# Optimization experiments

Hardware: AMD Instinct MI355X
Metric: run time of the kernel (lower is better)

The kernel has to match this reference:

```python
import jax, jax.numpy as jnp
import numpy as np
from jax import lax

D_MODEL, D_INNER, D_CONV, D_STATE, DT_RANK = 1024, 2048, 4, 16, 64
B, L = 2, 1024


def setup_inputs() -> dict:
    key = jax.random.key(0)
    ks = jax.random.split(key, 10)
    s = 0.02
    return {
        "x": jax.random.normal(ks[0], (B, L, D_MODEL), jnp.float32),
        "in_proj_w": jax.random.normal(ks[1], (2 * D_INNER, D_MODEL), jnp.float32) * s,
        "conv_w": jax.random.normal(ks[2], (D_INNER, 1, D_CONV), jnp.float32) * 0.1,
        "conv_b": jax.random.normal(ks[3], (D_INNER,), jnp.float32) * s,
        "x_proj_w": jax.random.normal(ks[4], (DT_RANK + 2 * D_STATE, D_INNER), jnp.float32) * s,
        "dt_proj_w": jax.random.normal(ks[5], (D_INNER, DT_RANK), jnp.float32) * s,
        "dt_proj_b": jax.random.normal(ks[6], (D_INNER,), jnp.float32) * s,
        "A_log": jnp.log(jnp.broadcast_to(jnp.arange(1, D_STATE + 1, dtype=jnp.float32), (D_INNER, D_STATE))),
        "D": jax.random.normal(ks[7], (D_INNER,), jnp.float32),
        "out_proj_w": jax.random.normal(ks[8], (D_MODEL, D_INNER), jnp.float32) * s,
    }


def _silu(v):
    return v * jax.nn.sigmoid(v)


def reference(x, in_proj_w, conv_w, conv_b, x_proj_w, dt_proj_w, dt_proj_b, A_log, D, out_proj_w):
    # in_proj: [B,L,d_model] -> [B,L,2*d_inner], split into x and gate z
    xz = jnp.einsum("bld,ed->ble", x, in_proj_w)
    xi, z = jnp.split(xz, 2, axis=-1)  # each [B,L,d_inner]

    # depthwise causal conv1d (padding = d_conv-1 on the left, output length L)
    xc = jnp.transpose(xi, (0, 2, 1))  # [B, d_inner, L]
    xc = lax.conv_general_dilated(
        xc, conv_w, window_strides=(1,), padding=[(D_CONV - 1, 0)],
        feature_group_count=D_INNER, dimension_numbers=("NCH", "OIH", "NCH"))
    xc = xc + conv_b[None, :, None]
    xc = _silu(jnp.transpose(xc, (0, 2, 1)))  # [B,L,d_inner]

    # selective scan parameters
    x_dbl = jnp.einsum("bld,ed->ble", xc, x_proj_w)  # [B,L,dt_rank+2*d_state]
    dt, Bm, Cm = jnp.split(x_dbl, [DT_RANK, DT_RANK + D_STATE], axis=-1)
    delta = jax.nn.softplus(jnp.einsum("blr,dr->bld", dt, dt_proj_w) + dt_proj_b)  # [B,L,d_inner]
    A = -jnp.exp(A_log)  # [d_inner, d_state]

    deltaA = jnp.exp(delta[..., None] * A)                       # [B,L,d_inner,N]
    deltaBu = delta[..., None] * Bm[:, :, None, :] * xc[..., None]  # [B,L,d_inner,N]

    def step(h, inp):
        a, bu, c = inp
        h = a * h + bu                         # [B,d_inner,N]
        y = jnp.einsum("bdn,bn->bd", h, c)     # [B,d_inner]
        return h, y

    h0 = jnp.zeros((x.shape[0], D_INNER, D_STATE), xc.dtype)
    _, ys = lax.scan(step, h0, (jnp.moveaxis(deltaA, 1, 0),
                                jnp.moveaxis(deltaBu, 1, 0),
                                jnp.moveaxis(Cm, 1, 0)))
    y = jnp.moveaxis(ys, 0, 1)  # [B,L,d_inner]

    y = y + xc * D
    y = y * _silu(z)
    return jnp.einsum("bld,ed->ble", y, out_proj_w)  # [B,L,d_model]
```

## Files before the change

kernel.cpp:

```cpp
#include <hip/hip_runtime.h>
#include <math.h>
#include <stdint.h>

#define DMODEL 1024
#define DINNER 2048
#define DCONV  4
#define DSTATE 16
#define DTRANK 64
#define BB 2
#define LL 1024
#define MM (BB * LL)

#define CL  64
#define NCH (LL / CL)

#define AS1(p) ((__attribute__((address_space(1))) void*)(void*)(p))
#define AS3(p) ((__attribute__((address_space(3))) void*)(void*)(p))

typedef __attribute__((ext_vector_type(8))) short bf16x8;
typedef __attribute__((ext_vector_type(4))) float f32x4;

__device__ __forceinline__ ushort bf16_rne(float f) {
  uint32_t u = __float_as_uint(f);
  uint32_t r = (u + 0x7fffu + ((u >> 16) & 1u)) >> 16;
  return (ushort)r;
}

__device__ __forceinline__ void split4(const float* __restrict__ in,
                                       ushort* __restrict__ hi,
                                       ushort* __restrict__ lo, int i4) {
  const float4 v = *reinterpret_cast<const float4*>(in + (size_t)i4 * 4);
  ushort4 h;
  h.x = bf16_rne(v.x); h.y = bf16_rne(v.y);
  h.z = bf16_rne(v.z); h.w = bf16_rne(v.w);
  *reinterpret_cast<ushort4*>(hi + (size_t)i4 * 4) = h;
  if (lo) {
    ushort4 l;
    l.x = bf16_rne(v.x - __uint_as_float((uint)h.x << 16));
    l.y = bf16_rne(v.y - __uint_as_float((uint)h.y << 16));
    l.z = bf16_rne(v.z - __uint_as_float((uint)h.z << 16));
    l.w = bf16_rne(v.w - __uint_as_float((uint)h.w << 16));
    *reinterpret_cast<ushort4*>(lo + (size_t)i4 * 4) = l;
  }
}

__global__ __launch_bounds__(256)
void split3(const float* s0, ushort* h0, ushort* l0, int n0,
            const float* s1, ushort* h1, ushort* l1, int n1,
            const float* s2, ushort* h2, ushort* l2, int n2,
            const float* s3, ushort* h3, ushort* l3, int n3) {
  int i = blockIdx.x * 256 + threadIdx.x;
  if (i < n0) { split4(s0, h0, l0, i); return; }
  i -= n0;
  if (i < n1) { split4(s1, h1, l1, i); return; }
  i -= n1;
  if (i < n2) { split4(s2, h2, l2, i); return; }
  i -= n2;
  if (i < n3) { split4(s3, h3, l3, i); return; }
}

__device__ __forceinline__ int swz4(int r) { return (r & 3) ^ ((r >> 2) & 3); }

template<int EPI, int SPLITK>
__global__ __launch_bounds__(256)
void gemm_hl_mfma(const ushort* __restrict__ Ahg, const ushort* __restrict__ Alg,
                  const ushort* __restrict__ Bhg, const ushort* __restrict__ Blg,
                  float* __restrict__ C, const float* __restrict__ bias,
                  int M, int N, int K) {
  __shared__ ushort Ah[2][128][32];
  __shared__ ushort Al[2][128][32];
  __shared__ ushort Bh[2][128][32];
  __shared__ ushort Bl[2][128][32];

  const int tid  = threadIdx.x;
  const int wave = tid >> 6;
  const int lane = tid & 63;
  const int m0 = blockIdx.y * 128;
  const int n0 = blockIdx.x * 128;
  const int wm = (wave >> 1) * 64;
  const int wn = (wave & 1) * 64;

  const int ksl = K / SPLITK;
  const int kb  = blockIdx.z * ksl;
  float* Cout   = C + (size_t)blockIdx.z * M * N;

  f32x4 acc[4][4];
  #pragma unroll
  for (int i = 0; i < 4; ++i)
    #pragma unroll
    for (int j = 0; j < 4; ++j)
      acc[i][j] = (f32x4){0.f, 0.f, 0.f, 0.f};

  const ushort* gsrc; ushort* dst; int row0;
  if      (wave == 0) { gsrc = Ahg; dst = &Ah[0][0][0]; row0 = m0; }
  else if (wave == 1) { gsrc = Alg; dst = &Al[0][0][0]; row0 = m0; }
  else if (wave == 2) { gsrc = Bhg; dst = &Bh[0][0][0]; row0 = n0; }
  else                { gsrc = Blg; dst = &Bl[0][0][0]; row0 = n0; }

  const int lr = lane >> 2;
  const int ls = lane & 3;
  const int fr = lane & 15;
  const int q  = lane >> 4;

  auto STAGE = [&](int bi, int k0) {
    ushort* d = dst + bi * 4096;
    #pragma unroll
    for (int seg = 0; seg < 8; ++seg) {
      const int rho = seg * 16 + lr;
      const int ks  = (ls ^ swz4(rho)) * 8;
      __builtin_amdgcn_global_load_lds(
          AS1(gsrc + (size_t)(row0 + rho) * K + k0 + ks),
          AS3(d + seg * 512), 16, 0, 0);
    }
  };

  const int NT = ksl / 32;
  STAGE(0, kb);
  __syncthreads();

  int cur = 0;
  for (int kt = 0; kt < NT; ++kt) {
    if (kt + 1 < NT) STAGE(cur ^ 1, kb + (kt + 1) * 32);

    bf16x8 ah[4], al[4], bh[4], bl[4];
    #pragma unroll
    for (int f = 0; f < 4; ++f) {
      { const int r = wm + f * 16 + fr; const int s = 8 * (q ^ swz4(r));
        ah[f] = *reinterpret_cast<const bf16x8*>(&Ah[cur][r][s]);
        al[f] = *reinterpret_cast<const bf16x8*>(&Al[cur][r][s]); }
      { const int r = wn + f * 16 + fr; const int s = 8 * (q ^ swz4(r));
        bh[f] = *reinterpret_cast<const bf16x8*>(&Bh[cur][r][s]);
        bl[f] = *reinterpret_cast<const bf16x8*>(&Bl[cur][r][s]); }
    }
    #pragma unroll
    for (int i = 0; i < 4; ++i)
      #pragma unroll
      for (int j = 0; j < 4; ++j) {
        acc[i][j] = __builtin_amdgcn_mfma_f32_16x16x32_bf16(ah[i], bh[j], acc[i][j], 0, 0, 0);
        acc[i][j] = __builtin_amdgcn_mfma_f32_16x16x32_bf16(al[i], bh[j], acc[i][j], 0, 0, 0);
        acc[i][j] = __builtin_amdgcn_mfma_f32_16x16x32_bf16(ah[i], bl[j], acc[i][j], 0, 0, 0);
      }

    __syncthreads();
    cur ^= 1;
  }

  const int cr = (lane >> 4) * 4;
  const int cc = lane & 15;
  #pragma unroll
  for (int i = 0; i < 4; ++i)
    #pragma unroll
    for (int j = 0; j < 4; ++j) {
      const int cn = n0 + wn + j * 16 + cc;
      const float bj = (EPI == 1) ? bias[cn] : 0.f;
      const size_t base = (size_t)(m0 + wm + i * 16 + cr) * N + cn;
      #pragma unroll
      for (int r = 0; r < 4; ++r) {
        float v = acc[i][j][r];
        if (EPI == 1) {
          v += bj;
          v = fmaxf(v, 0.f) + __logf(1.f + __expf(-fabsf(v)));
        }
        Cout[base + (size_t)r * N] = v;
      }
    }
}

template<int EPI, int SPLITK>
__global__ __launch_bounds__(256)
void gemm_p1_mfma(const ushort* __restrict__ Ahg, const ushort* __restrict__ Bhg,
                  float* __restrict__ P, int M, int N, int K) {
  __shared__ ushort Ah[2][128][32];
  __shared__ ushort Bh[2][128][32];

  const int tid  = threadIdx.x;
  const int wave = tid >> 6;
  const int lane = tid & 63;
  const int m0 = blockIdx.y * 128;
  const int n0 = blockIdx.x * 128;
  const int wm = (wave >> 1) * 64;
  const int wn = (wave & 1) * 64;

  const int ksl = K / SPLITK;
  const int kb  = blockIdx.z * ksl;
  float* Cout   = P + (size_t)blockIdx.z * M * N;

  f32x4 acc[4][4];
  #pragma unroll
  for (int i = 0; i < 4; ++i)
    #pragma unroll
    for (int j = 0; j < 4; ++j)
      acc[i][j] = (f32x4){0.f, 0.f, 0.f, 0.f};

  const ushort* gsrc = nullptr; ushort* dst = nullptr; int row0 = 0;
  if      (wave == 0) { gsrc = Ahg; dst = &Ah[0][0][0]; row0 = m0; }
  else if (wave == 1) { gsrc = Bhg; dst = &Bh[0][0][0]; row0 = n0; }

  const int lr = lane >> 2;
  const int ls = lane & 3;
  const int fr = lane & 15;
  const int q  = lane >> 4;

  auto STAGE = [&](int bi, int k0) {
    if (wave >= 2) return;
    ushort* d = dst + bi * 4096;
    #pragma unroll
    for (int seg = 0; seg < 8; ++seg) {
      const int rho = seg * 16 + lr;
      const int ks  = (ls ^ swz4(rho)) * 8;
      __builtin_amdgcn_global_load_lds(
          AS1(gsrc + (size_t)(row0 + rho) * K + k0 + ks),
          AS3(d + seg * 512), 16, 0, 0);
    }
  };

  const int NT = ksl / 32;
  STAGE(0, kb);
  __syncthreads();

  int cur = 0;
  for (int kt = 0; kt < NT; ++kt) {
    if (kt + 1 < NT) STAGE(cur ^ 1, kb + (kt + 1) * 32);

    bf16x8 ah[4], bh[4];
    #pragma unroll
    for (int f = 0; f < 4; ++f) {
      { const int r = wm + f * 16 + fr; const int s = 8 * (q ^ swz4(r));
        ah[f] = *reinterpret_cast<const bf16x8*>(&Ah[cur][r][s]); }
      { const int r = wn + f * 16 + fr; const int s = 8 * (q ^ swz4(r));
        bh[f] = *reinterpret_cast<const bf16x8*>(&Bh[cur][r][s]); }
    }
    #pragma unroll
    for (int i = 0; i < 4; ++i)
      #pragma unroll
      for (int j = 0; j < 4; ++j)
        acc[i][j] = __builtin_amdgcn_mfma_f32_16x16x32_bf16(ah[i], bh[j], acc[i][j], 0, 0, 0);

    __syncthreads();
    cur ^= 1;
  }

  const int cr = (lane >> 4) * 4;
  const int cc = lane & 15;
  #pragma unroll
  for (int i = 0; i < 4; ++i)
    #pragma unroll
    for (int j = 0; j < 4; ++j) {
      const int cn = n0 + wn + j * 16 + cc;
      const size_t base = (size_t)(m0 + wm + i * 16 + cr) * N + cn;
      #pragma unroll
      for (int r = 0; r < 4; ++r) {
        float v = acc[i][j][r];
        if (EPI == 2 && cn >= DINNER)
          v = v / (1.f + __expf(-v));
        Cout[base + (size_t)r * N] = v;
      }
    }
}

__global__ __launch_bounds__(256)
void splitk_reduce4(const float* __restrict__ P, float* __restrict__ out, int n) {
  const int i = (blockIdx.x * 256 + threadIdx.x) * 4;
  if (i >= n) return;
  float4 s = *reinterpret_cast<const float4*>(P + i);
  #pragma unroll
  for (int z = 1; z < 4; ++z) {
    const float4 v = *reinterpret_cast<const float4*>(P + (size_t)z * n + i);
    s.x += v.x; s.y += v.y; s.z += v.z; s.w += v.w;
  }
  *reinterpret_cast<float4*>(out + i) = s;
}

template<int BM, int BN, int TM, int TN, int KSLICE>
__global__ __launch_bounds__(256)
void gemm_nt_part(const float* __restrict__ A, const float* __restrict__ Bw,
                  float* __restrict__ P, int M, int N, int lda, int ldb) {
  constexpr int BK  = 16;
  constexpr int NTX = BN / TN;
  constexpr int NTY = BM / TM;
  static_assert(NTX * NTY == 256, "thread tile mismatch");
  __shared__ float As[BK][BM + 4];
  __shared__ float Bs[BK][BN + 4];

  const int tid = threadIdx.x;
  const int m0  = blockIdx.y * BM;
  const int n0  = blockIdx.x * BN;
  const int kb  = blockIdx.z * KSLICE;
  const int tx  = tid % NTX;
  const int ty  = tid / NTX;

  float acc[TM][TN] = {};

  for (int k0 = kb; k0 < kb + KSLICE; k0 += BK) {
    __syncthreads();
    for (int t = tid; t < BM * 4; t += 256) {
      const int row = t >> 2, kq = t & 3;
      const float4 v = *reinterpret_cast<const float4*>(
          A + (size_t)(m0 + row) * lda + k0 + kq * 4);
      As[kq * 4 + 0][row] = v.x;
      As[kq * 4 + 1][row] = v.y;
      As[kq * 4 + 2][row] = v.z;
      As[kq * 4 + 3][row] = v.w;
    }
    for (int t = tid; t < BN * 4; t += 256) {
      const int row = t >> 2, kq = t & 3;
      const float4 v = *reinterpret_cast<const float4*>(
          Bw + (size_t)(n0 + row) * ldb + k0 + kq * 4);
      Bs[kq * 4 + 0][row] = v.x;
      Bs[kq * 4 + 1][row] = v.y;
      Bs[kq * 4 + 2][row] = v.z;
      Bs[kq * 4 + 3][row] = v.w;
    }
    __syncthreads();
    #pragma unroll
    for (int k = 0; k < BK; ++k) {
      float a[TM], b[TN];
      #pragma unroll
      for (int i = 0; i < TM; ++i) a[i] = As[k][ty * TM + i];
      #pragma unroll
      for (int j = 0; j < TN; ++j) b[j] = Bs[k][tx * TN + j];
      #pragma unroll
      for (int i = 0; i < TM; ++i)
        #pragma unroll
        for (int j = 0; j < TN; ++j)
          acc[i][j] = fmaf(a[i], b[j], acc[i][j]);
    }
  }

  float* out = P + (size_t)blockIdx.z * M * N;
  #pragma unroll
  for (int i = 0; i < TM; ++i)
    #pragma unroll
    for (int j = 0; j < TN; ++j)
      out[(size_t)(m0 + ty * TM + i) * N + n0 + tx * TN + j] = acc[i][j];
}

__global__ __launch_bounds__(256)
void xpr_fused(const float* __restrict__ part, float* __restrict__ xdbl,
               ushort* __restrict__ dth, ushort* __restrict__ dtl) {
  const int i = blockIdx.x * 256 + threadIdx.x;
  if (i >= MM * 24) return;
  const int m  = i / 24;
  const int c4 = (i % 24) * 4;
  const size_t off = (size_t)m * 96 + c4;
  float4 s = *reinterpret_cast<const float4*>(part + off);
  #pragma unroll
  for (int z = 1; z < 8; ++z) {
    const float4 v = *reinterpret_cast<const float4*>(part + (size_t)z * MM * 96 + off);
    s.x += v.x; s.y += v.y; s.z += v.z; s.w += v.w;
  }
  if (c4 < 64) {
    ushort4 h, l;
    h.x = bf16_rne(s.x); l.x = bf16_rne(s.x - __uint_as_float((uint)h.x << 16));
    h.y = bf16_rne(s.y); l.y = bf16_rne(s.y - __uint_as_float((uint)h.y << 16));
    h.z = bf16_rne(s.z); l.z = bf16_rne(s.z - __uint_as_float((uint)h.z << 16));
    h.w = bf16_rne(s.w); l.w = bf16_rne(s.w - __uint_as_float((uint)h.w << 16));
    *reinterpret_cast<ushort4*>(dth + (size_t)m * 64 + c4) = h;
    *reinterpret_cast<ushort4*>(dtl + (size_t)m * 64 + c4) = l;
  } else {
    *reinterpret_cast<float4*>(xdbl + off) = s;
  }
}

__global__ __launch_bounds__(256)
void conv_silu(const float* __restrict__ xz, const float* __restrict__ cw,
               const float* __restrict__ cb, float* __restrict__ xc) {
  const int idx = blockIdx.x * 256 + threadIdx.x;
  if (idx >= MM * DINNER / 4) return;
  const int d4 = (idx & 511) * 4;
  const int m  = idx >> 9;
  const int l  = m & (LL - 1);
  const int b  = m >> 10;

  float4 w0 = *reinterpret_cast<const float4*>(cw + (size_t)(d4 + 0) * 4);
  float4 w1 = *reinterpret_cast<const float4*>(cw + (size_t)(d4 + 1) * 4);
  float4 w2 = *reinterpret_cast<const float4*>(cw + (size_t)(d4 + 2) * 4);
  float4 w3 = *reinterpret_cast<const float4*>(cw + (size_t)(d4 + 3) * 4);
  float4 acc = *reinterpret_cast<const float4*>(cb + d4);

  #pragma unroll
  for (int j = 0; j < DCONV; ++j) {
    const int ll = l - (DCONV - 1) + j;
    if (ll >= 0) {
      const float4 xv = *reinterpret_cast<const float4*>(
          xz + ((size_t)(b * LL + ll) << 12) + d4);
      acc.x = fmaf(xv.x, (&w0.x)[j], acc.x);
      acc.y = fmaf(xv.y, (&w1.x)[j], acc.y);
      acc.z = fmaf(xv.z, (&w2.x)[j], acc.z);
      acc.w = fmaf(xv.w, (&w3.x)[j], acc.w);
    }
  }
  float4 o;
  o.x = acc.x / (1.f + __expf(-acc.x));
  o.y = acc.y / (1.f + __expf(-acc.y));
  o.z = acc.z / (1.f + __expf(-acc.z));
  o.w = acc.w / (1.f + __expf(-acc.w));
  *reinterpret_cast<float4*>(xc + (size_t)m * DINNER + d4) = o;
}

__device__ __forceinline__ void stage_tile(const float* g, int stride,
                                           float* ldst, int lane) {
  const int r  = lane >> 2;
  const int q4 = (lane & 3) * 4;
  #pragma unroll
  for (int i = 0; i < 4; ++i) {
    __builtin_amdgcn_global_load_lds(
        AS1(g + (size_t)(i * 16 + r) * stride + q4),
        AS3(ldst + i * 256), 16, 0, 0);
  }
}

__device__ __forceinline__ float quad_sum(float v) {
  int i = __float_as_int(v);
  v += __int_as_float(__builtin_amdgcn_update_dpp(0, i, 0xB1, 0xf, 0xf, true));
  i = __float_as_int(v);
  v += __int_as_float(__builtin_amdgcn_update_dpp(0, i, 0x4E, 0xf, 0xf, true));
  return v;
}

__global__ __launch_bounds__(64)
void scan_chunk_state(const float* __restrict__ delta, const float* __restrict__ xc,
                      const float* __restrict__ xdbl, const float* __restrict__ A_log,
                      float* __restrict__ hend, float* __restrict__ aprod) {
  __shared__ float dT[CL][16];
  __shared__ float xT[CL][16];
  __shared__ float bT[CL][16];

  const int idx = blockIdx.x;
  const int c  = idx & 15;
  const int dg = (idx >> 4) & 127;
  const int b  = idx >> 11;
  const int t  = threadIdx.x;
  const int ch = t >> 2;
  const int q  = t & 3;
  const int d  = dg * 16 + ch;

  const size_t r0 = (size_t)b * LL + (size_t)c * CL;
  stage_tile(delta + r0 * DINNER + dg * 16, DINNER, &dT[0][0], t);
  stage_tile(xc    + r0 * DINNER + dg * 16, DINNER, &xT[0][0], t);
  stage_tile(xdbl  + r0 * 96 + DTRANK,          96, &bT[0][0], t);

  float Adn[4];
  #pragma unroll
  for (int j = 0; j < 4; ++j)
    Adn[j] = -__expf(A_log[d * DSTATE + 4 * q + j]);
  float h0 = 0.f, h1 = 0.f, h2 = 0.f, h3 = 0.f;
  float p0 = 1.f, p1 = 1.f, p2 = 1.f, p3 = 1.f;

  __syncthreads();

  #pragma unroll 8
  for (int l = 0; l < CL; ++l) {
    const float dv = dT[l][ch];
    const float xv = xT[l][ch];
    const float4 B4 = *reinterpret_cast<const float4*>(&bT[l][4 * q]);
    const float dvx = dv * xv;
    const float a0 = __expf(dv * Adn[0]);
    const float a1 = __expf(dv * Adn[1]);
    const float a2 = __expf(dv * Adn[2]);
    const float a3 = __expf(dv * Adn[3]);
    h0 = fmaf(a0, h0, dvx * B4.x);  p0 *= a0;
    h1 = fmaf(a1, h1, dvx * B4.y);  p1 *= a1;
    h2 = fmaf(a2, h2, dvx * B4.z);  p2 *= a2;
    h3 = fmaf(a3, h3, dvx * B4.w);  p3 *= a3;
  }

  const size_t base = (((size_t)(b * NCH + c) * DINNER) + d) * DSTATE + 4 * q;
  *reinterpret_cast<float4*>(hend  + base) = (float4){h0, h1, h2, h3};
  *reinterpret_cast<float4*>(aprod + base) = (float4){p0, p1, p2, p3};
}

__global__ __launch_bounds__(256)
void scan_combine(const float* __restrict__ hend, const float* __restrict__ aprod,
                  float* __restrict__ hin) {
  const int tid = blockIdx.x * 256 + threadIdx.x;
  const size_t cstride = (size_t)DINNER * DSTATE;
  const size_t base = (size_t)(tid >> 15) * NCH * cstride + (tid & 32767);
  float h = 0.f;
  hin[base] = 0.f;
  #pragma unroll
  for (int c = 0; c < NCH - 1; ++c) {
    h = fmaf(aprod[base + (size_t)c * cstride], h, hend[base + (size_t)c * cstride]);
    hin[base + (size_t)(c + 1) * cstride] = h;
  }
}

__global__ __launch_bounds__(64)
void scan_apply(const float* __restrict__ delta, const float* __restrict__ xc,
                const float* __restrict__ xdbl, const float* __restrict__ xz,
                const float* __restrict__ A_log, const float* __restrict__ Dp,
                const float* __restrict__ hin, ushort* __restrict__ yh) {
  __shared__ float dT[CL][16];
  __shared__ float xT[CL][16];
  __shared__ float bT[CL][16];
  __shared__ float cT[CL][16];
  __shared__ float zT[CL][16];

  const int idx = blockIdx.x;
  const int c  = idx & 15;
  const int dg = (idx >> 4) & 127;
  const int b  = idx >> 11;
  const int t  = threadIdx.x;
  const int ch = t >> 2;
  const int q  = t & 3;
  const int d  = dg * 16 + ch;

  const size_t r0 = (size_t)b * LL + (size_t)c * CL;
  stage_tile(delta + r0 * DINNER + dg * 16, DINNER, &dT[0][0], t);
  stage_tile(xc    + r0 * DINNER + dg * 16, DINNER, &xT[0][0], t);
  stage_tile(xdbl  + r0 * 96 + DTRANK,          96, &bT[0][0], t);
  stage_tile(xdbl  + r0 * 96 + DTRANK + DSTATE, 96, &cT[0][0], t);
  stage_tile(xz    + (r0 << 12) + DINNER + dg * 16, 4096, &zT[0][0], t);

  float Adn[4];
  #pragma unroll
  for (int j = 0; j < 4; ++j)
    Adn[j] = -__expf(A_log[d * DSTATE + 4 * q + j]);
  const float Dd = Dp[d];

  const size_t base = (((size_t)(b * NCH + c) * DINNER) + d) * DSTATE + 4 * q;
  const float4 h4 = *reinterpret_cast<const float4*>(hin + base);
  float h0 = h4.x, h1 = h4.y, h2 = h4.z, h3 = h4.w;

  __syncthreads();

  #pragma unroll 8
  for (int l = 0; l < CL; ++l) {
    const float dv = dT[l][ch];
    const float xv = xT[l][ch];
    const float4 B4 = *reinterpret_cast<const float4*>(&bT[l][4 * q]);
    const float4 C4 = *reinterpret_cast<const float4*>(&cT[l][4 * q]);
    const float dvx = dv * xv;
    const float a0 = __expf(dv * Adn[0]);
    const float a1 = __expf(dv * Adn[1]);
    const float a2 = __expf(dv * Adn[2]);
    const float a3 = __expf(dv * Adn[3]);
    h0 = fmaf(a0, h0, dvx * B4.x);
    h1 = fmaf(a1, h1, dvx * B4.y);
    h2 = fmaf(a2, h2, dvx * B4.z);
    h3 = fmaf(a3, h3, dvx * B4.w);
    float ys = fmaf(h0, C4.x, fmaf(h1, C4.y, fmaf(h2, C4.z, h3 * C4.w)));
    ys = quad_sum(ys);
    if (q == 0) {
      const float g = zT[l][ch];
      const float tv = (ys + xv * Dd) * g;
      yh[(r0 + l) * (size_t)DINNER + d] = bf16_rne(tv);
    }
  }
}

extern "C" void kernel_launch(void* const* d_in, const int* in_sizes, int n_in,
                              void* d_out, int out_size, void* d_ws, size_t ws_size,
                              hipStream_t stream) {
  const float* x         = (const float*)d_in[0];
  const float* in_proj_w = (const float*)d_in[1];
  const float* conv_w    = (const float*)d_in[2];
  const float* conv_b    = (const float*)d_in[3];
  const float* x_proj_w  = (const float*)d_in[4];
  const float* dt_proj_w = (const float*)d_in[5];
  const float* dt_proj_b = (const float*)d_in[6];
  const float* A_log     = (const float*)d_in[7];
  const float* Dv        = (const float*)d_in[8];
  const float* out_proj_w= (const float*)d_in[9];
  float* out = (float*)d_out;

  float* ws    = (float*)d_ws;
  float* xz    = ws;
  float* xc    = xz    + (size_t)MM * 4096;
  float* xdbl  = xc    + (size_t)MM * DINNER;
  float* delta = xdbl  + (size_t)MM * 96;
  ushort* us   = (ushort*)(delta + (size_t)MM * DINNER);
  ushort* yhp  = us;
  ushort* ylp  = yhp + (size_t)MM * DINNER;
  ushort* xh   = ylp + (size_t)MM * DINNER;
  ushort* xl   = xh  + (size_t)MM * DMODEL;
  ushort* wih  = xl  + (size_t)MM * DMODEL;
  ushort* wil  = wih + (size_t)4096 * DMODEL;
  ushort* woh  = wil + (size_t)4096 * DMODEL;

  ushort* dth = ylp;
  ushort* dtl = ylp + 131072;
  ushort* wdh = ylp + 262144;
  ushort* wdl = ylp + 393216;

  float* hend  = (float*)wih;
  float* aprod = hend  + (size_t)BB * NCH * DINNER * DSTATE;
  float* hin   = aprod + (size_t)BB * NCH * DINNER * DSTATE;
  float* part  = hend;
  float* opart = xz;

  const dim3 blk(256);

  {
    const int n0 = (MM * DMODEL) / 4, n1 = (4096 * DMODEL) / 4,
              n2 = (DMODEL * DINNER) / 4, n3 = (DINNER * DTRANK) / 4;
    split3<<<dim3((n0 + n1 + n2 + n3) / 256), blk, 0, stream>>>(
        x, xh, nullptr, n0, in_proj_w, wih, nullptr, n1,
        out_proj_w, woh, nullptr, n2, dt_proj_w, wdh, wdl, n3);
  }

  gemm_p1_mfma<2,1><<<dim3(4096 / 128, MM / 128), blk, 0, stream>>>(
      xh, wih, xz, MM, 4096, DMODEL);

  conv_silu<<<dim3((MM * DINNER / 4) / 256), blk, 0, stream>>>(xz, conv_w, conv_b, xc);

  gemm_nt_part<64,32,4,2,256><<<dim3(96/32, MM/64, 8), blk, 0, stream>>>(
      xc, x_proj_w, part, MM, 96, DINNER, DINNER);
  xpr_fused<<<dim3((MM * 24 + 255) / 256), blk, 0, stream>>>(part, xdbl, dth, dtl);

  gemm_hl_mfma<1,1><<<dim3(DINNER / 128, MM / 128), blk, 0, stream>>>(
      dth, dtl, wdh, wdl, delta, dt_proj_b, MM, DINNER, DTRANK);

  scan_chunk_state<<<dim3(BB * 128 * NCH), dim3(64), 0, stream>>>(
      delta, xc, xdbl, A_log, hend, aprod);
  scan_combine<<<dim3(BB * DINNER * DSTATE / 256), blk, 0, stream>>>(
      hend, aprod, hin);
  scan_apply<<<dim3(BB * 128 * NCH), dim3(64), 0, stream>>>(
      delta, xc, xdbl, xz, A_log, Dv, hin, yhp);

  gemm_p1_mfma<0,4><<<dim3(DMODEL / 128, MM / 128, 4), blk, 0, stream>>>(
      yhp, woh, opart, MM, DMODEL, DINNER);
  splitk_reduce4<<<dim3((MM * DMODEL) / 1024), blk, 0, stream>>>(
      opart, out, MM * DMODEL);
}
```

Measured before the change: 167.5 us.

## Store in_proj output as bf16 and coalesce GEMM epilogue via LDS transpose

The in_proj GEMM now writes its xz result as bf16 instead of fp32, halving the bytes written and later read by conv_silu and scan_apply. scan_apply stages the gate tile straight into LDS with global_load_lds. The GEMM epilogue now goes through shared memory so each lane writes contiguous float4 or ushort4 rows instead of scattered scalars, and the silu branch is decided per block. The cost is lost precision in xi and z, which now carry bf16 rounding into the conv and gating, plus extra LDS traffic in the epilogue.

```diff
diff --git a/kernel.cpp b/kernel.cpp
--- a/kernel.cpp
+++ b/kernel.cpp
@@ -24,6 +24,9 @@
   uint32_t u = __float_as_uint(f);
   uint32_t r = (u + 0x7fffu + ((u >> 16) & 1u)) >> 16;
   return (ushort)r;
+}
+__device__ __forceinline__ float bf2f(ushort u) {
+  return __uint_as_float((uint32_t)u << 16);
 }
 
 __device__ __forceinline__ void split4(const float* __restrict__ in,
@@ -36,10 +39,10 @@
   *reinterpret_cast<ushort4*>(hi + (size_t)i4 * 4) = h;
   if (lo) {
     ushort4 l;
-    l.x = bf16_rne(v.x - __uint_as_float((uint)h.x << 16));
-    l.y = bf16_rne(v.y - __uint_as_float((uint)h.y << 16));
-    l.z = bf16_rne(v.z - __uint_as_float((uint)h.z << 16));
-    l.w = bf16_rne(v.w - __uint_as_float((uint)h.w << 16));
+    l.x = bf16_rne(v.x - bf2f(h.x));
+    l.y = bf16_rne(v.y - bf2f(h.y));
+    l.z = bf16_rne(v.z - bf2f(h.z));
+    l.w = bf16_rne(v.w - bf2f(h.w));
     *reinterpret_cast<ushort4*>(lo + (size_t)i4 * 4) = l;
   }
 }
@@ -166,12 +169,12 @@
     }
 }
 
-template<int EPI, int SPLITK>
+template<int EPI, int SPLITK, bool OBF16>
 __global__ __launch_bounds__(256)
 void gemm_p1_mfma(const ushort* __restrict__ Ahg, const ushort* __restrict__ Bhg,
-                  float* __restrict__ P, int M, int N, int K) {
-  __shared__ ushort Ah[2][128][32];
-  __shared__ ushort Bh[2][128][32];
+                  float* __restrict__ Pf, ushort* __restrict__ Pb,
+                  int M, int N, int K) {
+  __shared__ ushort smem[16384];
 
   const int tid  = threadIdx.x;
   const int wave = tid >> 6;
@@ -183,7 +186,6 @@
 
   const int ksl = K / SPLITK;
   const int kb  = blockIdx.z * ksl;
-  float* Cout   = P + (size_t)blockIdx.z * M * N;
 
   f32x4 acc[4][4];
   #pragma unroll
@@ -193,8 +195,8 @@
       acc[i][j] = (f32x4){0.f, 0.f, 0.f, 0.f};
 
   const ushort* gsrc = nullptr; ushort* dst = nullptr; int row0 = 0;
-  if      (wave == 0) { gsrc = Ahg; dst = &Ah[0][0][0]; row0 = m0; }
-  else if (wave == 1) { gsrc = Bhg; dst = &Bh[0][0][0]; row0 = n0; }
+  if      (wave == 0) { gsrc = Ahg; dst = smem;        row0 = m0; }
+  else if (wave == 1) { gsrc = Bhg; dst = smem + 8192; row0 = n0; }
 
   const int lr = lane >> 2;
   const int ls = lane & 3;
@@ -226,9 +228,9 @@
     #pragma unroll
     for (int f = 0; f < 4; ++f) {
       { const int r = wm + f * 16 + fr; const int s = 8 * (q ^ swz4(r));
-        ah[f] = *reinterpret_cast<const bf16x8*>(&Ah[cur][r][s]); }
+        ah[f] = *reinterpret_cast<const bf16x8*>(&smem[cur * 4096 + r * 32 + s]); }
       { const int r = wn + f * 16 + fr; const int s = 8 * (q ^ swz4(r));
-        bh[f] = *reinterpret_cast<const bf16x8*>(&Bh[cur][r][s]); }
+        bh[f] = *reinterpret_cast<const bf16x8*>(&smem[8192 + cur * 4096 + r * 32 + s]); }
     }
     #pragma unroll
     for (int i = 0; i < 4; ++i)
@@ -240,22 +242,46 @@
     cur ^= 1;
   }
 
+  float* T = reinterpret_cast<float*>(smem) + wave * 2048;
   const int cr = (lane >> 4) * 4;
   const int cc = lane & 15;
-  #pragma unroll
-  for (int i = 0; i < 4; ++i)
-    #pragma unroll
-    for (int j = 0; j < 4; ++j) {
-      const int cn = n0 + wn + j * 16 + cc;
-      const size_t base = (size_t)(m0 + wm + i * 16 + cr) * N + cn;
+  const bool do_silu = (EPI == 2) && (n0 >= DINNER);
+
+  #pragma unroll
+  for (int p = 0; p < 2; ++p) {
+    #pragma unroll
+    for (int ii = 0; ii < 2; ++ii) {
+      const int i = 2 * p + ii;
       #pragma unroll
-      for (int r = 0; r < 4; ++r) {
-        float v = acc[i][j][r];
-        if (EPI == 2 && cn >= DINNER)
-          v = v / (1.f + __expf(-v));
-        Cout[base + (size_t)r * N] = v;
+      for (int j = 0; j < 4; ++j)
+        #pragma unroll
+        for (int r = 0; r < 4; ++r)
+          T[(ii * 16 + cr + r) * 64 + j * 16 + cc] = acc[i][j][r];
+    }
+    #pragma unroll
+    for (int rr = 0; rr < 8; ++rr) {
+      const int row  = rr * 4 + (lane >> 4);
+      const int col4 = (lane & 15) * 4;
+      float4 v = *reinterpret_cast<const float4*>(&T[row * 64 + col4]);
+      const size_t grow = (size_t)(m0 + wm + p * 32 + row);
+      const int    gcol = n0 + wn + col4;
+      if (do_silu) {
+        v.x = v.x / (1.f + __expf(-v.x));
+        v.y = v.y / (1.f + __expf(-v.y));
+        v.z = v.z / (1.f + __expf(-v.z));
+        v.w = v.w / (1.f + __expf(-v.w));
       }
-    }
+      if (OBF16) {
+        ushort4 h;
+        h.x = bf16_rne(v.x); h.y = bf16_rne(v.y);
+        h.z = bf16_rne(v.z); h.w = bf16_rne(v.w);
+        *reinterpret_cast<ushort4*>(Pb + grow * N + gcol) = h;
+      } else {
+        float* Cout = Pf + (size_t)blockIdx.z * M * N;
+        *reinterpret_cast<float4*>(Cout + grow * N + gcol) = v;
+      }
+    }
+  }
 }
 
 __global__ __launch_bounds__(256)
@@ -351,10 +377,10 @@
   }
   if (c4 < 64) {
     ushort4 h, l;
-    h.x = bf16_rne(s.x); l.x = bf16_rne(s.x - __uint_as_float((uint)h.x << 16));
-    h.y = bf16_rne(s.y); l.y = bf16_rne(s.y - __uint_as_float((uint)h.y << 16));
-    h.z = bf16_rne(s.z); l.z = bf16_rne(s.z - __uint_as_float((uint)h.z << 16));
-    h.w = bf16_rne(s.w); l.w = bf16_rne(s.w - __uint_as_float((uint)h.w << 16));
+    h.x = bf16_rne(s.x); l.x = bf16_rne(s.x - bf2f(h.x));
+    h.y = bf16_rne(s.y); l.y = bf16_rne(s.y - bf2f(h.y));
+    h.z = bf16_rne(s.z); l.z = bf16_rne(s.z - bf2f(h.z));
+    h.w = bf16_rne(s.w); l.w = bf16_rne(s.w - bf2f(h.w));
     *reinterpret_cast<ushort4*>(dth + (size_t)m * 64 + c4) = h;
     *reinterpret_cast<ushort4*>(dtl + (size_t)m * 64 + c4) = l;
   } else {
@@ -363,7 +389,7 @@
 }
 
 __global__ __launch_bounds__(256)
-void conv_silu(const float* __restrict__ xz, const float* __restrict__ cw,
+void conv_silu(const ushort* __restrict__ xzb, const float* __restrict__ cw,
                const float* __restrict__ cb, float* __restrict__ xc) {
   const int idx = blockIdx.x * 256 + threadIdx.x;
   if (idx >= MM * DINNER / 4) return;
@@ -382,12 +408,12 @@
   for (int j = 0; j < DCONV; ++j) {
     const int ll = l - (DCONV - 1) + j;
     if (ll >= 0) {
-      const float4 xv = *reinterpret_cast<const float4*>(
-          xz + ((size_t)(b * LL + ll) << 12) + d4);
-      acc.x = fmaf(xv.x, (&w0.x)[j], acc.x);
-      acc.y = fmaf(xv.y, (&w1.x)[j], acc.y);
-      acc.z = fmaf(xv.z, (&w2.x)[j], acc.z);
-      acc.w = fmaf(xv.w, (&w3.x)[j], acc.w);
+      const ushort4 xv = *reinterpret_cast<const ushort4*>(
+          xzb + ((size_t)(b * LL + ll) << 12) + d4);
+      acc.x = fmaf(bf2f(xv.x), (&w0.x)[j], acc.x);
+      acc.y = fmaf(bf2f(xv.y), (&w1.x)[j], acc.y);
+      acc.z = fmaf(bf2f(xv.z), (&w2.x)[j], acc.z);
+      acc.w = fmaf(bf2f(xv.w), (&w3.x)[j], acc.w);
     }
   }
   float4 o;
@@ -487,14 +513,14 @@
 
 __global__ __launch_bounds__(64)
 void scan_apply(const float* __restrict__ delta, const float* __restrict__ xc,
-                const float* __restrict__ xdbl, const float* __restrict__ xz,
+                const float* __restrict__ xdbl, const ushort* __restrict__ xzb,
                 const float* __restrict__ A_log, const float* __restrict__ Dp,
                 const float* __restrict__ hin, ushort* __restrict__ yh) {
-  __shared__ float dT[CL][16];
-  __shared__ float xT[CL][16];
-  __shared__ float bT[CL][16];
-  __shared__ float cT[CL][16];
-  __shared__ float zT[CL][16];
+  __shared__ float  dT[CL][16];
+  __shared__ float  xT[CL][16];
+  __shared__ float  bT[CL][16];
+  __shared__ float  cT[CL][16];
+  __shared__ ushort zT[CL][16];
 
   const int idx = blockIdx.x;
   const int c  = idx & 15;
@@ -510,7 +536,17 @@
   stage_tile(xc    + r0 * DINNER + dg * 16, DINNER, &xT[0][0], t);
   stage_tile(xdbl  + r0 * 96 + DTRANK,          96, &bT[0][0], t);
   stage_tile(xdbl  + r0 * 96 + DTRANK + DSTATE, 96, &cT[0][0], t);
-  stage_tile(xz    + (r0 << 12) + DINNER + dg * 16, 4096, &zT[0][0], t);
+  {
+    const ushort* g = xzb + (r0 << 12) + DINNER + dg * 16;
+    const int r  = t >> 1;
+    const int h8 = (t & 1) * 8;
+    #pragma unroll
+    for (int i = 0; i < 2; ++i) {
+      __builtin_amdgcn_global_load_lds(
+          AS1(g + (size_t)(i * 32 + r) * 4096 + h8),
+          AS3(&zT[0][0] + i * 512), 16, 0, 0);
+    }
+  }
 
   float Adn[4];
   #pragma unroll
@@ -542,7 +578,7 @@
     float ys = fmaf(h0, C4.x, fmaf(h1, C4.y, fmaf(h2, C4.z, h3 * C4.w)));
     ys = quad_sum(ys);
     if (q == 0) {
-      const float g = zT[l][ch];
+      const float g = bf2f(zT[l][ch]);
       const float tv = (ys + xv * Dd) * g;
       yh[(r0 + l) * (size_t)DINNER + d] = bf16_rne(tv);
     }
@@ -578,6 +614,8 @@
   ushort* wil  = wih + (size_t)4096 * DMODEL;
   ushort* woh  = wil + (size_t)4096 * DMODEL;
 
+  ushort* xzb = (ushort*)xz;
+
   ushort* dth = ylp;
   ushort* dtl = ylp + 131072;
   ushort* wdh = ylp + 262144;
@@ -599,10 +637,10 @@
         out_proj_w, woh, nullptr, n2, dt_proj_w, wdh, wdl, n3);
   }
 
-  gemm_p1_mfma<2,1><<<dim3(4096 / 128, MM / 128), blk, 0, stream>>>(
-      xh, wih, xz, MM, 4096, DMODEL);
-
-  conv_silu<<<dim3((MM * DINNER / 4) / 256), blk, 0, stream>>>(xz, conv_w, conv_b, xc);
+  gemm_p1_mfma<2, 1, true><<<dim3(4096 / 128, MM / 128), blk, 0, stream>>>(
+      xh, wih, nullptr, xzb, MM, 4096, DMODEL);
+
+  conv_silu<<<dim3((MM * DINNER / 4) / 256), blk, 0, stream>>>(xzb, conv_w, conv_b, xc);
 
   gemm_nt_part<64,32,4,2,256><<<dim3(96/32, MM/64, 8), blk, 0, stream>>>(
       xc, x_proj_w, part, MM, 96, DINNER, DINNER);
@@ -616,10 +654,10 @@
   scan_combine<<<dim3(BB * DINNER * DSTATE / 256), blk, 0, stream>>>(
       hend, aprod, hin);
   scan_apply<<<dim3(BB * 128 * NCH), dim3(64), 0, stream>>>(
-      delta, xc, xdbl, xz, A_log, Dv, hin, yhp);
-
-  gemm_p1_mfma<0,4><<<dim3(DMODEL / 128, MM / 128, 4), blk, 0, stream>>>(
-      yhp, woh, opart, MM, DMODEL, DINNER);
+      delta, xc, xdbl, xzb, A_log, Dv, hin, yhp);
+
+  gemm_p1_mfma<0, 4, false><<<dim3(DMODEL / 128, MM / 128, 4), blk, 0, stream>>>(
+      yhp, woh, opart, nullptr, MM, DMODEL, DINNER);
   splitk_reduce4<<<dim3((MM * DMODEL) / 1024), blk, 0, stream>>>(
       opart, out, MM * DMODEL);
 }
```

After: 167.4 us. About the same (-0.0%).
